# Kernel optimization log

Hardware: AMD Instinct MI355X
Metric: run time of the kernel (lower is better)

The kernel has to match this reference:

```python
import jax, jax.numpy as jnp
import numpy as np

B, N, F = 16, 20000, 512

def setup_inputs() -> dict:
    key = jax.random.key(0)
    k1, k2 = jax.random.split(key)
    input_data = jax.random.normal(k1, (B, N, F), dtype=jnp.float32)
    # he_normal init for kernel (fan_in = F)
    kernel = jax.random.normal(k2, (F, 1), dtype=jnp.float32) * jnp.sqrt(2.0 / F)
    return {"input_data": input_data, "kernel": kernel, "select_dim": 200}

def reference(input_data, kernel, select_dim):
    # score: [B, N, 1]
    scores = jnp.einsum('bnf,fo->bno', input_data, kernel)
    probs = jax.nn.softmax(scores, axis=1)            # softmax over features axis
    flat = probs[..., 0]                              # [B, N]
    _, top_idx = jax.lax.top_k(flat, select_dim)      # [B, k]
    # batched gathers (tf.gather with batch_dims=1)
    emb = jnp.take_along_axis(input_data, top_idx[..., None], axis=1)  # [B, k, F]
    sel = jnp.take_along_axis(probs, top_idx[..., None], axis=1)       # [B, k, 1]
    sel = jax.nn.softmax(sel, axis=1)                 # re-softmax over selected
    summed = jnp.sum(emb * sel, axis=1)               # [B, F]
    # tf.math.l2_normalize with axis=None: normalize by global L2 norm
    out_emb = summed * jax.lax.rsqrt(jnp.maximum(jnp.sum(summed * summed), 1e-12))
    return top_idx.astype(jnp.int32), probs, out_emb
```

## Files before the change

### kernel.cpp

```cpp
#include <hip/hip_runtime.h>
#include <hip/hip_bf16.h>

#define B 16
#define N 20000
#define F 512
#define K 200
#define ROWS (B*N)
#define CH 10
#define RPC 20
#define CAP 2048

__device__ __forceinline__ unsigned key32(float s){
    unsigned u = __float_as_uint(s);
    return (u & 0x80000000u) ? ~u : (u | 0x80000000u);
}
__device__ __forceinline__ float inv_key32(unsigned k){
    unsigned u = (k & 0x80000000u) ? (k & 0x7FFFFFFFu) : ~k;
    return __uint_as_float(u);
}
__device__ __forceinline__ unsigned long long key64(double s){
    unsigned long long u = (unsigned long long)__double_as_longlong(s);
    return (u >> 63) ? ~u : (u | 0x8000000000000000ull);
}

__global__ void k_init(unsigned* bmax){
    if (threadIdx.x < B) bmax[threadIdx.x] = 0u;
}

__global__ __launch_bounds__(256) void k_scores(const float* __restrict__ x,
                                                const float* __restrict__ w,
                                                double* __restrict__ sc,
                                                unsigned* __restrict__ bmax,
                                                int rows_per_block){
    __shared__ unsigned lmax[B];
    int t = threadIdx.x;
    if (t < B) lmax[t] = 0u;
    __syncthreads();
    int lane = t & 63, wid = t >> 6;

    const float4* w4 = (const float4*)w;
    float4 ka = w4[lane*2], kb = w4[lane*2+1];
    double k0=ka.x,k1=ka.y,k2=ka.z,k3=ka.w,k4=kb.x,k5=kb.y,k6=kb.z,k7=kb.w;

    long seg = (long)blockIdx.x * rows_per_block;
    long end = seg + rows_per_block; if (end > (long)ROWS) end = ROWS;
    for (long r = seg + wid; r < end; r += 4){
        const float4* rp = (const float4*)(x + r*(long)F);
        float4 a = rp[lane*2], b2 = rp[lane*2+1];
        double acc = (double)a.x*k0 + (double)a.y*k1 + (double)a.z*k2 + (double)a.w*k3
                   + (double)b2.x*k4 + (double)b2.y*k5 + (double)b2.z*k6 + (double)b2.w*k7;
        #pragma unroll
        for (int m=1; m<64; m<<=1) acc += __shfl_xor(acc, m, 64);
        if (lane == 0){
            sc[r] = acc;
            int b = (int)(r / N);
            atomicMax(&lmax[b], key32((float)acc));
        }
    }
    __syncthreads();
    if (t < B && lmax[t]) atomicMax(&bmax[t], lmax[t]);
}

__global__ __launch_bounds__(1024) void k_sumexp(const double* __restrict__ sc,
                                                 const unsigned* __restrict__ bmax,
                                                 double* __restrict__ bsum){
    __shared__ double red[1024];
    int b = blockIdx.x, t = threadIdx.x;
    float m = inv_key32(bmax[b]);
    const double* s = sc + (long)b*N;
    double acc = 0.0;
    for (int n = t; n < N; n += 1024) acc += (double)expf((float)s[n] - m);
    red[t] = acc; __syncthreads();
    for (int o = 512; o > 0; o >>= 1){ if (t < o) red[t] += red[t+o]; __syncthreads(); }
    if (t == 0) bsum[b] = red[0];
}

__global__ __launch_bounds__(1024) void k_topk(const double* __restrict__ sc,
                                               const unsigned* __restrict__ bmax,
                                               const double* __restrict__ bsum,
                                               float* __restrict__ out,
                                               int* __restrict__ selidx,
                                               float* __restrict__ selw){
    __shared__ unsigned hist[2048];
    __shared__ unsigned long long ckey[CAP];
    __shared__ int cidx[CAP];
    __shared__ float selp[256];
    __shared__ float fred[1024];
    __shared__ int ccount, pivot;

    int b = blockIdx.x, t = threadIdx.x;
    const double* s = sc + (long)b*N;
    float m = inv_key32(bmax[b]);
    float sumf = (float)bsum[b];

    hist[t] = 0u; hist[t+1024] = 0u;
    if (t == 0) ccount = 0;
    __syncthreads();

    float* probs_out = out + B*K + (long)b*N;
    for (int n = t; n < N; n += 1024){
        float sf = (float)s[n];
        atomicAdd(&hist[key32(sf)>>21], 1u);
        probs_out[n] = expf(sf - m) / sumf;
    }
    __syncthreads();

    for (int off = 1; off < 2048; off <<= 1){
        unsigned v0 = hist[t]      + ((t+off)      < 2048 ? hist[t+off]      : 0u);
        unsigned v1 = hist[t+1024] + ((t+1024+off) < 2048 ? hist[t+1024+off] : 0u);
        __syncthreads();
        hist[t] = v0; hist[t+1024] = v1;
        __syncthreads();
    }
    for (int tt = t; tt < 2048; tt += 1024){
        if (hist[tt] >= K && (tt == 2047 || hist[tt+1] < K)) pivot = tt;
    }
    __syncthreads();
    int P = pivot;

    for (int n = t; n < N; n += 1024){
        float sf = (float)s[n];
        if ((int)(key32(sf)>>21) >= P){
            int pos = atomicAdd(&ccount, 1);
            if (pos < CAP){ ckey[pos] = key64(s[n]); cidx[pos] = n; }
        }
    }
    __syncthreads();
    int C = ccount; if (C > CAP) C = CAP;

    for (int i = t; i < C; i += 1024){
        unsigned long long ki = ckey[i]; int xi = cidx[i];
        int rank = 0;
        for (int j = 0; j < C; j++){
            unsigned long long kj = ckey[j];
            rank += (kj > ki) || (kj == ki && cidx[j] < xi);
        }
        if (rank < K){
            out[b*K + rank] = (float)xi;
            selidx[b*K + rank] = xi;
            float sf = (float)s[xi];
            selp[rank] = expf(sf - m) / sumf;
        }
    }
    __syncthreads();

    float v = (t < K) ? selp[t] : -3.0e38f;
    fred[t] = v; __syncthreads();
    for (int o = 512; o > 0; o >>= 1){ if (t < o) fred[t] = fmaxf(fred[t], fred[t+o]); __syncthreads(); }
    float m2 = fred[0]; __syncthreads();
    float wv = (t < K) ? expf(selp[t] - m2) : 0.0f;
    fred[t] = wv; __syncthreads();
    for (int o = 512; o > 0; o >>= 1){ if (t < o) fred[t] += fred[t+o]; __syncthreads(); }
    float sw = fred[0];
    if (t < K) selw[b*K + t] = wv / sw;
}

__global__ __launch_bounds__(128) void k_gather(const float* __restrict__ x,
                                                const int* __restrict__ selidx,
                                                const float* __restrict__ selw,
                                                float* __restrict__ partial){
    int b = blockIdx.x / CH, ch = blockIdx.x % CH;
    int t = threadIdx.x;
    float4 acc = {0.f,0.f,0.f,0.f};
    for (int i = 0; i < RPC; i++){
        int s = b*K + ch*RPC + i;
        int idx = selidx[s];
        float wv = selw[s];
        const float4* rp = (const float4*)(x + ((long)b*N + idx)*(long)F);
        float4 vv = rp[t];
        acc.x += wv*vv.x; acc.y += wv*vv.y; acc.z += wv*vv.z; acc.w += wv*vv.w;
    }
    float4* pp = (float4*)(partial + (long)(b*CH + ch)*F);
    pp[t] = acc;
}

__global__ __launch_bounds__(1024) void k_final(const float* __restrict__ partial,
                                                float* __restrict__ out_emb){
    __shared__ double red[1024];
    int t = threadIdx.x;
    float mine[8];
    double ssq = 0.0;
    #pragma unroll
    for (int k = 0; k < 8; k++){
        int i = t + k*1024;
        int b = i >> 9, f = i & 511;
        float sv = 0.f;
        for (int c = 0; c < CH; c++) sv += partial[(b*CH + c)*F + f];
        mine[k] = sv;
        ssq += (double)sv * sv;
    }
    red[t] = ssq; __syncthreads();
    for (int o = 512; o > 0; o >>= 1){ if (t < o) red[t] += red[t+o]; __syncthreads(); }
    float scale = rsqrtf(fmaxf((float)red[0], 1e-12f));
    #pragma unroll
    for (int k = 0; k < 8; k++){
        int i = t + k*1024;
        out_emb[i] = mine[k] * scale;
    }
}

extern "C" void kernel_launch(void* const* d_in, const int* in_sizes, int n_in,
                              void* d_out, int out_size, void* d_ws, size_t ws_size,
                              hipStream_t stream){
    const float* x = (const float*)d_in[0];
    const float* w = (const float*)d_in[1];
    float* out = (float*)d_out;
    char* ws = (char*)d_ws;

    double*   sc      = (double*)(ws);
    unsigned* bmax    = (unsigned*)(ws + 2560000);
    double*   bsum    = (double*)(ws + 2560064);
    int*      selidx  = (int*)(ws + 2560192);
    float*    selw    = (float*)(ws + 2572992);
    float*    partial = (float*)(ws + 2585792);

    k_init<<<dim3(1), dim3(64), 0, stream>>>(bmax);

    const int grid1 = 2048;
    const int rpb = (ROWS + grid1 - 1) / grid1;
    k_scores<<<dim3(grid1), dim3(256), 0, stream>>>(x, w, sc, bmax, rpb);

    k_sumexp<<<dim3(B), dim3(1024), 0, stream>>>(sc, bmax, bsum);

    k_topk<<<dim3(B), dim3(1024), 0, stream>>>(sc, bmax, bsum, out, selidx, selw);

    k_gather<<<dim3(B*CH), dim3(128), 0, stream>>>(x, selidx, selw, partial);

    k_final<<<dim3(1), dim3(1024), 0, stream>>>(partial, out + B*K + (long)B*N);
}
```

Before: 208.1 us.

## Fuse softmax sum into scores pass and merge topk, gather, reduce kernels

Removes the per-batch max and computes the exp sum directly in the scores kernel as per-block partial sums, dropping the k_init and k_sumexp launches and the extra pass over the scores. The scores loop now prefetches the next rows and processes two rows per wave at a time. Top-k, softmax weights and the weighted gather are merged into one kernel per batch, with the gather reduced in shared memory. Skipping max subtraction risks exp overflow for large scores, and the gather now runs on only 16 blocks instead of 160.

After: 201.0 us. 1.04x faster.

```diff
diff --git a/kernel.cpp b/kernel.cpp
--- a/kernel.cpp
+++ b/kernel.cpp
@@ -6,102 +6,104 @@
 #define F 512
 #define K 200
 #define ROWS (B*N)
-#define CH 10
-#define RPC 20
+#define GRID1 2000
+#define RPB 160
+#define PSB 125
 #define CAP 2048
 
 __device__ __forceinline__ unsigned key32(float s){
     unsigned u = __float_as_uint(s);
     return (u & 0x80000000u) ? ~u : (u | 0x80000000u);
 }
-__device__ __forceinline__ float inv_key32(unsigned k){
-    unsigned u = (k & 0x80000000u) ? (k & 0x7FFFFFFFu) : ~k;
-    return __uint_as_float(u);
-}
 __device__ __forceinline__ unsigned long long key64(double s){
     unsigned long long u = (unsigned long long)__double_as_longlong(s);
     return (u >> 63) ? ~u : (u | 0x8000000000000000ull);
 }
-
-__global__ void k_init(unsigned* bmax){
-    if (threadIdx.x < B) bmax[threadIdx.x] = 0u;
+__device__ __forceinline__ double inv_key64(unsigned long long k){
+    unsigned long long u = (k >> 63) ? (k & 0x7FFFFFFFFFFFFFFFull) : ~k;
+    return __longlong_as_double((long long)u);
 }
 
 __global__ __launch_bounds__(256) void k_scores(const float* __restrict__ x,
                                                 const float* __restrict__ w,
                                                 double* __restrict__ sc,
-                                                unsigned* __restrict__ bmax,
-                                                int rows_per_block){
-    __shared__ unsigned lmax[B];
-    int t = threadIdx.x;
-    if (t < B) lmax[t] = 0u;
-    __syncthreads();
-    int lane = t & 63, wid = t >> 6;
+                                                double* __restrict__ psum){
+    __shared__ double wsum[4];
+    int t = threadIdx.x, lane = t & 63, wid = t >> 6;
 
     const float4* w4 = (const float4*)w;
     float4 ka = w4[lane*2], kb = w4[lane*2+1];
     double k0=ka.x,k1=ka.y,k2=ka.z,k3=ka.w,k4=kb.x,k5=kb.y,k6=kb.z,k7=kb.w;
 
-    long seg = (long)blockIdx.x * rows_per_block;
-    long end = seg + rows_per_block; if (end > (long)ROWS) end = ROWS;
-    for (long r = seg + wid; r < end; r += 4){
-        const float4* rp = (const float4*)(x + r*(long)F);
-        float4 a = rp[lane*2], b2 = rp[lane*2+1];
-        double acc = (double)a.x*k0 + (double)a.y*k1 + (double)a.z*k2 + (double)a.w*k3
-                   + (double)b2.x*k4 + (double)b2.y*k5 + (double)b2.z*k6 + (double)b2.w*k7;
+    const float4* xp = (const float4*)x;
+    long seg = (long)blockIdx.x * RPB;
+    long r0 = seg + wid;
+    double esum = 0.0;
+
+    float4 a0 = xp[r0*128 + lane*2],     a1 = xp[r0*128 + lane*2 + 1];
+    float4 b0 = xp[(r0+4)*128 + lane*2], b1 = xp[(r0+4)*128 + lane*2 + 1];
+
+    #pragma unroll 1
+    for (int it = 0; it < 20; ++it){
+        long r = r0 + (long)it*8;
+        float4 na0=a0, na1=a1, nb0=b0, nb1=b1;
+        if (it < 19){
+            long nr = r + 8;
+            na0 = xp[nr*128 + lane*2];     na1 = xp[nr*128 + lane*2 + 1];
+            nb0 = xp[(nr+4)*128 + lane*2]; nb1 = xp[(nr+4)*128 + lane*2 + 1];
+        }
+        double accA = (double)a0.x*k0 + (double)a0.y*k1 + (double)a0.z*k2 + (double)a0.w*k3
+                    + (double)a1.x*k4 + (double)a1.y*k5 + (double)a1.z*k6 + (double)a1.w*k7;
+        double accB = (double)b0.x*k0 + (double)b0.y*k1 + (double)b0.z*k2 + (double)b0.w*k3
+                    + (double)b1.x*k4 + (double)b1.y*k5 + (double)b1.z*k6 + (double)b1.w*k7;
         #pragma unroll
-        for (int m=1; m<64; m<<=1) acc += __shfl_xor(acc, m, 64);
+        for (int m=1; m<64; m<<=1){
+            accA += __shfl_xor(accA, m, 64);
+            accB += __shfl_xor(accB, m, 64);
+        }
         if (lane == 0){
-            sc[r] = acc;
-            int b = (int)(r / N);
-            atomicMax(&lmax[b], key32((float)acc));
-        }
-    }
-    __syncthreads();
-    if (t < B && lmax[t]) atomicMax(&bmax[t], lmax[t]);
-}
-
-__global__ __launch_bounds__(1024) void k_sumexp(const double* __restrict__ sc,
-                                                 const unsigned* __restrict__ bmax,
-                                                 double* __restrict__ bsum){
-    __shared__ double red[1024];
-    int b = blockIdx.x, t = threadIdx.x;
-    float m = inv_key32(bmax[b]);
-    const double* s = sc + (long)b*N;
-    double acc = 0.0;
-    for (int n = t; n < N; n += 1024) acc += (double)expf((float)s[n] - m);
-    red[t] = acc; __syncthreads();
-    for (int o = 512; o > 0; o >>= 1){ if (t < o) red[t] += red[t+o]; __syncthreads(); }
-    if (t == 0) bsum[b] = red[0];
-}
-
-__global__ __launch_bounds__(1024) void k_topk(const double* __restrict__ sc,
-                                               const unsigned* __restrict__ bmax,
-                                               const double* __restrict__ bsum,
-                                               float* __restrict__ out,
-                                               int* __restrict__ selidx,
-                                               float* __restrict__ selw){
+            sc[r]   = accA;
+            sc[r+4] = accB;
+            esum += (double)expf((float)accA) + (double)expf((float)accB);
+        }
+        a0=na0; a1=na1; b0=nb0; b1=nb1;
+    }
+    if (lane == 0) wsum[wid] = esum;
+    __syncthreads();
+    if (t == 0) psum[blockIdx.x] = ((wsum[0]+wsum[1]) + (wsum[2]+wsum[3]));
+}
+
+__global__ __launch_bounds__(1024) void k_fused(const double* __restrict__ sc,
+                                                const double* __restrict__ psum,
+                                                const float* __restrict__ x,
+                                                float* __restrict__ out,
+                                                float* __restrict__ summed){
     __shared__ unsigned hist[2048];
     __shared__ unsigned long long ckey[CAP];
     __shared__ int cidx[CAP];
     __shared__ float selp[256];
+    __shared__ int selidx_s[256];
+    __shared__ float selw_s[256];
     __shared__ float fred[1024];
+    __shared__ double dred[256];
+    __shared__ float4 gacc[8][128];
     __shared__ int ccount, pivot;
 
     int b = blockIdx.x, t = threadIdx.x;
     const double* s = sc + (long)b*N;
-    float m = inv_key32(bmax[b]);
-    float sumf = (float)bsum[b];
-
+
+    if (t < 256) dred[t] = (t < PSB) ? psum[b*PSB + t] : 0.0;
     hist[t] = 0u; hist[t+1024] = 0u;
     if (t == 0) ccount = 0;
     __syncthreads();
+    for (int o = 128; o > 0; o >>= 1){ if (t < o) dred[t] += dred[t+o]; __syncthreads(); }
+    float invsum = 1.0f / (float)dred[0];
 
     float* probs_out = out + B*K + (long)b*N;
     for (int n = t; n < N; n += 1024){
         float sf = (float)s[n];
         atomicAdd(&hist[key32(sf)>>21], 1u);
-        probs_out[n] = expf(sf - m) / sumf;
+        probs_out[n] = expf(sf) * invsum;
     }
     __syncthreads();
 
@@ -119,10 +121,11 @@
     int P = pivot;
 
     for (int n = t; n < N; n += 1024){
-        float sf = (float)s[n];
+        double sv = s[n];
+        float sf = (float)sv;
         if ((int)(key32(sf)>>21) >= P){
             int pos = atomicAdd(&ccount, 1);
-            if (pos < CAP){ ckey[pos] = key64(s[n]); cidx[pos] = n; }
+            if (pos < CAP){ ckey[pos] = key64(sv); cidx[pos] = n; }
         }
     }
     __syncthreads();
@@ -137,9 +140,8 @@
         }
         if (rank < K){
             out[b*K + rank] = (float)xi;
-            selidx[b*K + rank] = xi;
-            float sf = (float)s[xi];
-            selp[rank] = expf(sf - m) / sumf;
+            selidx_s[rank] = xi;
+            selp[rank] = expf((float)inv_key64(ki)) * invsum;
         }
     }
     __syncthreads();
@@ -152,30 +154,40 @@
     fred[t] = wv; __syncthreads();
     for (int o = 512; o > 0; o >>= 1){ if (t < o) fred[t] += fred[t+o]; __syncthreads(); }
     float sw = fred[0];
-    if (t < K) selw[b*K + t] = wv / sw;
-}
-
-__global__ __launch_bounds__(128) void k_gather(const float* __restrict__ x,
-                                                const int* __restrict__ selidx,
-                                                const float* __restrict__ selw,
-                                                float* __restrict__ partial){
-    int b = blockIdx.x / CH, ch = blockIdx.x % CH;
-    int t = threadIdx.x;
+    if (t < K) selw_s[t] = wv / sw;
+    __syncthreads();
+
+    int g = t >> 7, q = t & 127;
     float4 acc = {0.f,0.f,0.f,0.f};
-    for (int i = 0; i < RPC; i++){
-        int s = b*K + ch*RPC + i;
-        int idx = selidx[s];
-        float wv = selw[s];
+    for (int i = g; i < K; i += 8){
+        int idx = selidx_s[i];
+        float wvi = selw_s[i];
         const float4* rp = (const float4*)(x + ((long)b*N + idx)*(long)F);
-        float4 vv = rp[t];
-        acc.x += wv*vv.x; acc.y += wv*vv.y; acc.z += wv*vv.z; acc.w += wv*vv.w;
-    }
-    float4* pp = (float4*)(partial + (long)(b*CH + ch)*F);
-    pp[t] = acc;
-}
-
-__global__ __launch_bounds__(1024) void k_final(const float* __restrict__ partial,
-                                                float* __restrict__ out_emb){
+        float4 vv = rp[q];
+        acc.x += wvi*vv.x; acc.y += wvi*vv.y; acc.z += wvi*vv.z; acc.w += wvi*vv.w;
+    }
+    gacc[g][q] = acc; __syncthreads();
+    if (g < 4){
+        float4 o4 = gacc[g+4][q];
+        gacc[g][q].x += o4.x; gacc[g][q].y += o4.y; gacc[g][q].z += o4.z; gacc[g][q].w += o4.w;
+    }
+    __syncthreads();
+    if (g < 2){
+        float4 o4 = gacc[g+2][q];
+        gacc[g][q].x += o4.x; gacc[g][q].y += o4.y; gacc[g][q].z += o4.z; gacc[g][q].w += o4.w;
+    }
+    __syncthreads();
+    if (g == 0){
+        float4 o4 = gacc[1][q];
+        float4 r4 = gacc[0][q];
+        r4.x += o4.x; r4.y += o4.y; r4.z += o4.z; r4.w += o4.w;
+        float4* sp = (float4*)(summed + b*F);
+        sp[q] = r4;
+    }
+}
+
+__global__ __launch_bounds__(1024) void k_norm(const float* __restrict__ summed,
+                                               float* __restrict__ out_emb){
     __shared__ double red[1024];
     int t = threadIdx.x;
     float mine[8];
@@ -183,9 +195,7 @@
     #pragma unroll
     for (int k = 0; k < 8; k++){
         int i = t + k*1024;
-        int b = i >> 9, f = i & 511;
-        float sv = 0.f;
-        for (int c = 0; c < CH; c++) sv += partial[(b*CH + c)*F + f];
+        float sv = summed[i];
         mine[k] = sv;
         ssq += (double)sv * sv;
     }
@@ -207,24 +217,11 @@
     float* out = (float*)d_out;
     char* ws = (char*)d_ws;
 
-    double*   sc      = (double*)(ws);
-    unsigned* bmax    = (unsigned*)(ws + 2560000);
-    double*   bsum    = (double*)(ws + 2560064);
-    int*      selidx  = (int*)(ws + 2560192);
-    float*    selw    = (float*)(ws + 2572992);
-    float*    partial = (float*)(ws + 2585792);
-
-    k_init<<<dim3(1), dim3(64), 0, stream>>>(bmax);
-
-    const int grid1 = 2048;
-    const int rpb = (ROWS + grid1 - 1) / grid1;
-    k_scores<<<dim3(grid1), dim3(256), 0, stream>>>(x, w, sc, bmax, rpb);
-
-    k_sumexp<<<dim3(B), dim3(1024), 0, stream>>>(sc, bmax, bsum);
-
-    k_topk<<<dim3(B), dim3(1024), 0, stream>>>(sc, bmax, bsum, out, selidx, selw);
-
-    k_gather<<<dim3(B*CH), dim3(128), 0, stream>>>(x, selidx, selw, partial);
-
-    k_final<<<dim3(1), dim3(1024), 0, stream>>>(partial, out + B*K + (long)B*N);
-}
+    double* sc     = (double*)(ws);
+    double* psum   = (double*)(ws + 2560000);
+    float*  summed = (float*)(ws + 2576000);
+
+    k_scores<<<dim3(GRID1), dim3(256), 0, stream>>>(x, w, sc, psum);
+    k_fused<<<dim3(B), dim3(1024), 0, stream>>>(sc, psum, x, out, summed);
+    k_norm<<<dim3(1), dim3(1024), 0, stream>>>(summed, out + B*K + (long)B*N);
+}
```
